# Performance work log

Hardware: AMD Instinct MI355X
Metric: run time of the kernel (lower is better)

The kernel has to match this reference:

```python
import jax, jax.numpy as jnp
import numpy as np

P0 = 2   # tublet_size
P = 16   # patch_size
FC = 2   # flow channels (map_x, map_y)


def patchify(x, p0, p1, p2):
    # x: (B, C, T, H, W) -> (B, (T/p0)(H/p1)(W/p2), p0*p1*p2*C)
    B, C, T, H, W = x.shape
    x = x.reshape(B, C, T // p0, p0, H // p1, p1, W // p2, p2)
    x = x.transpose(0, 2, 4, 6, 3, 5, 7, 1)  # b t h w p0 p1 p2 c
    return x.reshape(B, (T // p0) * (H // p1) * (W // p2), p0 * p1 * p2 * C)


def unpatchify(x, p0, p1, p2, C, T, H, W):
    # x: (B, N, p0*p1*p2*C) -> (B, C, T, H, W)
    B = x.shape[0]
    x = x.reshape(B, T // p0, H // p1, W // p2, p0, p1, p2, C)
    x = x.transpose(0, 7, 1, 4, 2, 5, 3, 6)  # b c t p0 h p1 w p2
    return x.reshape(B, C, T, H, W)


def bilinear_warp(imgs, mx, my):
    # imgs: (B, C, T, H, W); mx, my: (B, T, H, W) absolute sample coords.
    # Equivalent of cv2.remap INTER_LINEAR with constant (zero) border.
    B, C, T, H, W = imgs.shape
    x0 = jnp.floor(mx)
    y0 = jnp.floor(my)
    wx = (mx - x0).reshape(B, 1, T, H * W)
    wy = (my - y0).reshape(B, 1, T, H * W)
    x0i = x0.astype(jnp.int32)
    y0i = y0.astype(jnp.int32)
    imgs_flat = imgs.reshape(B, C, T, H * W)

    def gather(yi, xi):
        yc = jnp.clip(yi, 0, H - 1)
        xc = jnp.clip(xi, 0, W - 1)
        idx = (yc * W + xc).reshape(B, 1, T, H * W)
        v = jnp.take_along_axis(imgs_flat, jnp.broadcast_to(idx, (B, C, T, H * W)), axis=-1)
        valid = ((yi >= 0) & (yi <= H - 1) & (xi >= 0) & (xi <= W - 1)).reshape(B, 1, T, H * W)
        return v * valid.astype(v.dtype)

    v00 = gather(y0i, x0i)
    v01 = gather(y0i, x0i + 1)
    v10 = gather(y0i + 1, x0i)
    v11 = gather(y0i + 1, x0i + 1)
    out = (v00 * (1 - wx) * (1 - wy) + v01 * wx * (1 - wy)
           + v10 * (1 - wx) * wy + v11 * wx * wy)
    return out.reshape(B, C, T, H, W)


def setup_inputs() -> dict:
    key = jax.random.key(0)
    k1, k2, k3 = jax.random.split(key, 3)
    B, C, T, H, W = 8, 3, 16, 224, 224
    N = (T // P0) * (H // P) * (W // P)         # 1568 tokens
    D = P0 * P * P * FC                         # 1024 per-token flow dim
    output = jax.random.normal(k1, (B, N, D), dtype=jnp.float32)
    raw_target = jax.random.normal(k2, (B, C, T, H, W), dtype=jnp.float32)
    mask = jax.random.randint(k3, (B, N), 0, 2) > 0
    return {"output": output, "raw_target": raw_target, "mask": mask}


def reference(output, raw_target, mask):
    B, C, T, H, W = raw_target.shape
    # tokens -> dense flow field (B, 2, T, H, W)
    flows = unpatchify(output, P0, P, P, FC, T, H, W)
    gx = jnp.arange(W, dtype=flows.dtype)               # (W,)
    gy = jnp.arange(H, dtype=flows.dtype)[:, None]      # (H, 1)
    mx = flows[:, 0] + gx                                # (B, T, H, W)
    my = flows[:, 1] + gy
    recons = bilinear_warp(raw_target, mx, my)           # (B, C, T, H, W)
    rec_p = patchify(recons, P0, P, P)                   # (B, N, p0*p1*p2*C)
    tgt_p = patchify(raw_target, P0, P, P)
    m = mask.astype(rec_p.dtype)[..., None]              # (B, N, 1)
    diff2 = (rec_p - tgt_p) ** 2 * m
    denom = jnp.maximum(m.sum(), 1.0) * rec_p.shape[-1]
    return diff2.sum() / denom
```

## Files before the change

kernel.cpp:

```cpp
#include <hip/hip_runtime.h>

#define Bd 8
#define Cd 3
#define Td 16
#define Hd 224
#define Wd 224
#define Nd 1568
#define Dd 1024
#define HWd (Hd*Wd)
#define TOTAL_PIX (Bd*Td*HWd)
#define MASK_N (Bd*Nd)
#define PATCH_ELEMS 1536.0
#define NBLK 2048

__global__ void flow_mse_partial(const float* __restrict__ outp,
                                 const float* __restrict__ raw,
                                 const int* __restrict__ mask,
                                 float* __restrict__ partial) {
    const int stride = gridDim.x * blockDim.x;
    float acc = 0.f;

    for (int g = blockIdx.x * blockDim.x + threadIdx.x; g < TOTAL_PIX; g += stride) {
        int bt  = g / HWd;
        int pix = g - bt * HWd;
        int b = bt >> 4;
        int t = bt & 15;
        int h = pix / Wd;
        int w = pix - h * Wd;

        int n = (t >> 1) * 196 + (h >> 4) * 14 + (w >> 4);

        if (mask[b * Nd + n] != 0) {
            size_t fbase = ((size_t)b * Nd + n) * Dd
                         + ((((t & 1) << 4) + (h & 15)) << 5)
                         + ((w & 15) << 1);
            float fx = outp[fbase];
            float fy = outp[fbase + 1];
            float mx = fx + (float)w;
            float my = fy + (float)h;

            float x0 = floorf(mx), y0 = floorf(my);
            float wx = mx - x0,    wy = my - y0;
            int x0i = (int)x0, y0i = (int)y0;
            int x1i = x0i + 1, y1i = y0i + 1;

            bool vx0 = (x0i >= 0) && (x0i < Wd);
            bool vx1 = (x1i >= 0) && (x1i < Wd);
            bool vy0 = (y0i >= 0) && (y0i < Hd);
            bool vy1 = (y1i >= 0) && (y1i < Hd);

            int xc0 = min(max(x0i, 0), Wd - 1);
            int xc1 = min(max(x1i, 0), Wd - 1);
            int yc0 = min(max(y0i, 0), Hd - 1);
            int yc1 = min(max(y1i, 0), Hd - 1);

            float w00 = (1.f - wx) * (1.f - wy) * ((vx0 && vy0) ? 1.f : 0.f);
            float w01 = wx         * (1.f - wy) * ((vx1 && vy0) ? 1.f : 0.f);
            float w10 = (1.f - wx) * wy         * ((vx0 && vy1) ? 1.f : 0.f);
            float w11 = wx         * wy         * ((vx1 && vy1) ? 1.f : 0.f);

            int i00 = yc0 * Wd + xc0;
            int i01 = yc0 * Wd + xc1;
            int i10 = yc1 * Wd + xc0;
            int i11 = yc1 * Wd + xc1;

            #pragma unroll
            for (int c = 0; c < Cd; ++c) {
                const float* img = raw + (((size_t)b * Cd + c) * Td + t) * HWd;
                float v00 = img[i00];
                float v01 = img[i01];
                float v10 = img[i10];
                float v11 = img[i11];
                float rec = v00 * w00 + v01 * w01 + v10 * w10 + v11 * w11;
                float tgt = img[h * Wd + w];
                float d = rec - tgt;
                acc += d * d;
            }
        }
    }

    for (int off = 32; off > 0; off >>= 1) acc += __shfl_down(acc, off, 64);
    __shared__ float sdata[4];
    int lane = threadIdx.x & 63, wid = threadIdx.x >> 6;
    if (lane == 0) sdata[wid] = acc;
    __syncthreads();
    if (threadIdx.x == 0) {
        partial[blockIdx.x] = sdata[0] + sdata[1] + sdata[2] + sdata[3];
    }
}

__global__ void finalize_kernel(const float* __restrict__ partial,
                                const int* __restrict__ mask,
                                float* __restrict__ out) {
    double s = 0.0;
    for (int i = threadIdx.x; i < NBLK; i += blockDim.x)
        s += (double)partial[i];
    int cnt = 0;
    for (int i = threadIdx.x; i < MASK_N; i += blockDim.x)
        cnt += (mask[i] != 0) ? 1 : 0;

    for (int off = 32; off > 0; off >>= 1) {
        s   += __shfl_down(s, off, 64);
        cnt += __shfl_down(cnt, off, 64);
    }
    __shared__ double sdat[4];
    __shared__ int    cdat[4];
    int lane = threadIdx.x & 63, wid = threadIdx.x >> 6;
    if (lane == 0) { sdat[wid] = s; cdat[wid] = cnt; }
    __syncthreads();
    if (threadIdx.x == 0) {
        double st = sdat[0] + sdat[1] + sdat[2] + sdat[3];
        int ct = cdat[0] + cdat[1] + cdat[2] + cdat[3];
        double denom = (double)(ct > 0 ? ct : 1) * PATCH_ELEMS;
        out[0] = (float)(st / denom);
    }
}

extern "C" void kernel_launch(void* const* d_in, const int* in_sizes, int n_in,
                              void* d_out, int out_size, void* d_ws, size_t ws_size,
                              hipStream_t stream) {
    const float* outp = (const float*)d_in[0];
    const float* raw  = (const float*)d_in[1];
    const int*   mask = (const int*)d_in[2];
    float* out = (float*)d_out;

    float* partial = (float*)d_ws;

    flow_mse_partial<<<NBLK, 256, 0, stream>>>(outp, raw, mask, partial);
    finalize_kernel<<<1, 256, 0, stream>>>(partial, mask, out);
}
```

Measured before the change: 191.7 us.

## Assign one block per token and skip masked tokens early

The grid-stride loop over pixels is replaced by one 256-thread block per token (B*N blocks). Each block exits at once when its mask bit is zero, so flow and image reads for unmasked tokens are skipped without any per-pixel mask checks. Flow values are read as contiguous float2, which coalesces better than the old pixel-order strided access. The finalize kernel now sums 12544 partials instead of 2048, and a single block has to walk that larger array serially.

Result: faster. 184.6 us (-3.7%).

```diff
diff --git a/kernel.cpp b/kernel.cpp
--- a/kernel.cpp
+++ b/kernel.cpp
@@ -8,92 +8,97 @@
 #define Nd 1568
 #define Dd 1024
 #define HWd (Hd*Wd)
-#define TOTAL_PIX (Bd*Td*HWd)
 #define MASK_N (Bd*Nd)
 #define PATCH_ELEMS 1536.0
-#define NBLK 2048
 
-__global__ void flow_mse_partial(const float* __restrict__ outp,
-                                 const float* __restrict__ raw,
-                                 const int* __restrict__ mask,
-                                 float* __restrict__ partial) {
-    const int stride = gridDim.x * blockDim.x;
+__global__ void flow_mse_tok(const float* __restrict__ outp,
+                             const float* __restrict__ raw,
+                             const int* __restrict__ mask,
+                             float* __restrict__ partial) {
+    const int tk = blockIdx.x;
+    const int tid = threadIdx.x;
+
+    if (mask[tk] == 0) {
+        if (tid == 0) partial[tk] = 0.f;
+        return;
+    }
+
+    const int b = tk / Nd;
+    const int n = tk - b * Nd;
+    const int t2  = n / 196;
+    const int rem = n - t2 * 196;
+    const int ph  = rem / 14;
+    const int pw  = rem - ph * 14;
+
+    const int i1 = tid >> 4;
+    const int i2 = tid & 15;
+    const int h = (ph << 4) + i1;
+    const int w = (pw << 4) + i2;
+
+    const float* fptr = outp + (size_t)tk * Dd;
+
     float acc = 0.f;
+    #pragma unroll
+    for (int i0 = 0; i0 < 2; ++i0) {
+        const int t = (t2 << 1) + i0;
+        float2 f = *(const float2*)(fptr + (((i0 << 8) + tid) << 1));
+        float mx = f.x + (float)w;
+        float my = f.y + (float)h;
 
-    for (int g = blockIdx.x * blockDim.x + threadIdx.x; g < TOTAL_PIX; g += stride) {
-        int bt  = g / HWd;
-        int pix = g - bt * HWd;
-        int b = bt >> 4;
-        int t = bt & 15;
-        int h = pix / Wd;
-        int w = pix - h * Wd;
+        float x0 = floorf(mx), y0 = floorf(my);
+        float wx = mx - x0,    wy = my - y0;
+        int x0i = (int)x0, y0i = (int)y0;
+        int x1i = x0i + 1, y1i = y0i + 1;
 
-        int n = (t >> 1) * 196 + (h >> 4) * 14 + (w >> 4);
+        bool vx0 = (x0i >= 0) && (x0i < Wd);
+        bool vx1 = (x1i >= 0) && (x1i < Wd);
+        bool vy0 = (y0i >= 0) && (y0i < Hd);
+        bool vy1 = (y1i >= 0) && (y1i < Hd);
 
-        if (mask[b * Nd + n] != 0) {
-            size_t fbase = ((size_t)b * Nd + n) * Dd
-                         + ((((t & 1) << 4) + (h & 15)) << 5)
-                         + ((w & 15) << 1);
-            float fx = outp[fbase];
-            float fy = outp[fbase + 1];
-            float mx = fx + (float)w;
-            float my = fy + (float)h;
+        int xc0 = min(max(x0i, 0), Wd - 1);
+        int xc1 = min(max(x1i, 0), Wd - 1);
+        int yc0 = min(max(y0i, 0), Hd - 1);
+        int yc1 = min(max(y1i, 0), Hd - 1);
 
-            float x0 = floorf(mx), y0 = floorf(my);
-            float wx = mx - x0,    wy = my - y0;
-            int x0i = (int)x0, y0i = (int)y0;
-            int x1i = x0i + 1, y1i = y0i + 1;
+        float w00 = (1.f - wx) * (1.f - wy) * ((vx0 && vy0) ? 1.f : 0.f);
+        float w01 = wx         * (1.f - wy) * ((vx1 && vy0) ? 1.f : 0.f);
+        float w10 = (1.f - wx) * wy         * ((vx0 && vy1) ? 1.f : 0.f);
+        float w11 = wx         * wy         * ((vx1 && vy1) ? 1.f : 0.f);
 
-            bool vx0 = (x0i >= 0) && (x0i < Wd);
-            bool vx1 = (x1i >= 0) && (x1i < Wd);
-            bool vy0 = (y0i >= 0) && (y0i < Hd);
-            bool vy1 = (y1i >= 0) && (y1i < Hd);
+        int i00 = yc0 * Wd + xc0;
+        int i01 = yc0 * Wd + xc1;
+        int i10 = yc1 * Wd + xc0;
+        int i11 = yc1 * Wd + xc1;
+        int itg = h * Wd + w;
 
-            int xc0 = min(max(x0i, 0), Wd - 1);
-            int xc1 = min(max(x1i, 0), Wd - 1);
-            int yc0 = min(max(y0i, 0), Hd - 1);
-            int yc1 = min(max(y1i, 0), Hd - 1);
-
-            float w00 = (1.f - wx) * (1.f - wy) * ((vx0 && vy0) ? 1.f : 0.f);
-            float w01 = wx         * (1.f - wy) * ((vx1 && vy0) ? 1.f : 0.f);
-            float w10 = (1.f - wx) * wy         * ((vx0 && vy1) ? 1.f : 0.f);
-            float w11 = wx         * wy         * ((vx1 && vy1) ? 1.f : 0.f);
-
-            int i00 = yc0 * Wd + xc0;
-            int i01 = yc0 * Wd + xc1;
-            int i10 = yc1 * Wd + xc0;
-            int i11 = yc1 * Wd + xc1;
-
-            #pragma unroll
-            for (int c = 0; c < Cd; ++c) {
-                const float* img = raw + (((size_t)b * Cd + c) * Td + t) * HWd;
-                float v00 = img[i00];
-                float v01 = img[i01];
-                float v10 = img[i10];
-                float v11 = img[i11];
-                float rec = v00 * w00 + v01 * w01 + v10 * w10 + v11 * w11;
-                float tgt = img[h * Wd + w];
-                float d = rec - tgt;
-                acc += d * d;
-            }
+        #pragma unroll
+        for (int c = 0; c < Cd; ++c) {
+            const float* img = raw + (size_t)(((b * Cd + c) * Td + t)) * HWd;
+            float v00 = img[i00];
+            float v01 = img[i01];
+            float v10 = img[i10];
+            float v11 = img[i11];
+            float rec = v00 * w00 + v01 * w01 + v10 * w10 + v11 * w11;
+            float tgt = img[itg];
+            float d = rec - tgt;
+            acc += d * d;
         }
     }
 
     for (int off = 32; off > 0; off >>= 1) acc += __shfl_down(acc, off, 64);
     __shared__ float sdata[4];
-    int lane = threadIdx.x & 63, wid = threadIdx.x >> 6;
+    int lane = tid & 63, wid = tid >> 6;
     if (lane == 0) sdata[wid] = acc;
     __syncthreads();
-    if (threadIdx.x == 0) {
-        partial[blockIdx.x] = sdata[0] + sdata[1] + sdata[2] + sdata[3];
-    }
+    if (tid == 0)
+        partial[tk] = sdata[0] + sdata[1] + sdata[2] + sdata[3];
 }
 
 __global__ void finalize_kernel(const float* __restrict__ partial,
                                 const int* __restrict__ mask,
                                 float* __restrict__ out) {
     double s = 0.0;
-    for (int i = threadIdx.x; i < NBLK; i += blockDim.x)
+    for (int i = threadIdx.x; i < MASK_N; i += blockDim.x)
         s += (double)partial[i];
     int cnt = 0;
     for (int i = threadIdx.x; i < MASK_N; i += blockDim.x)
@@ -126,6 +131,6 @@
 
     float* partial = (float*)d_ws;
 
-    flow_mse_partial<<<NBLK, 256, 0, stream>>>(outp, raw, mask, partial);
+    flow_mse_tok<<<MASK_N, 256, 0, stream>>>(outp, raw, mask, partial);
     finalize_kernel<<<1, 256, 0, stream>>>(partial, mask, out);
 }
```
